# Kernel tuning notes

Hardware: AMD Instinct MI355X
Metric: run time of the kernel (lower is better)

Reference implementation:

```python
import jax, jax.numpy as jnp
import numpy as np

B, S, D = 2, 2048, 1024
H, Dh = 16, 64  # qkv_features=1024, head_dim=64
F = 1024        # out_features


def setup_inputs() -> dict:
    key = jax.random.key(0)
    ks = jax.random.split(key, 16)
    s = 0.02
    return {
        'inputs_q': jax.random.normal(ks[0], (B, S, D), jnp.float32),
        'inputs_kv': jax.random.normal(ks[1], (B, S, D), jnp.float32),
        'pos_embed': jax.random.normal(ks[2], (S, D), jnp.float32),
        'Wq': jax.random.normal(ks[3], (D, H, Dh), jnp.float32) * s,
        'bq': jnp.zeros((H, Dh), jnp.float32),
        'Wk': jax.random.normal(ks[4], (D, H, Dh), jnp.float32) * s,
        'bk': jnp.zeros((H, Dh), jnp.float32),
        'Wv': jax.random.normal(ks[5], (D, H, Dh), jnp.float32) * s,
        'bv': jnp.zeros((H, Dh), jnp.float32),
        'Wpos': jax.random.normal(ks[6], (D, H, Dh), jnp.float32) * s,
        'r_r_bias': jax.random.normal(ks[7], (H, Dh), jnp.float32) * s,
        'r_w_bias': jax.random.normal(ks[8], (H, Dh), jnp.float32) * s,
        'Wout': jax.random.normal(ks[9], (H, Dh, F), jnp.float32) * s,
        'bout': jnp.zeros((F,), jnp.float32),
    }


_roll_vmap = jax.vmap(jnp.roll, in_axes=(-2, 0, None), out_axes=-2)


def reference(inputs_q, inputs_kv, pos_embed, Wq, bq, Wk, bk, Wv, bv,
              Wpos, r_r_bias, r_w_bias, Wout, bout):
    # QKV projections: [B,S,D] x [D,H,Dh] -> [B,S,H,Dh]
    q = jnp.einsum('bsd,dhk->bshk', inputs_q, Wq) + bq
    k = jnp.einsum('bsd,dhk->bshk', inputs_kv, Wk) + bk
    v = jnp.einsum('bsd,dhk->bshk', inputs_kv, Wv) + bv
    # relative position embedding projection: [S,D] -> [S,H,Dh]
    r_pos = jnp.einsum('sd,dhk->shk', pos_embed, Wpos)

    q_len = q.shape[-3]
    depth = q.shape[-1]
    # content score + relative-position score, both [B,H,S,S]
    aw = jnp.einsum('bqhd,bkhd->bhqk', q + r_w_bias, k)
    aw_r = jnp.einsum('bqhd,khd->bhqk', q + r_r_bias, r_pos)
    # Transformer-XL relative shift: per query-row roll along key axis
    shifts = jnp.arange(0, q_len) - (q_len - 1)
    aw_r = _roll_vmap(aw_r, shifts, -1)
    aw = (aw + aw_r) / jnp.sqrt(depth).astype(aw.dtype)
    attn = jax.nn.softmax(aw, axis=-1)
    # weighted sum: [B,S,H,Dh]
    x = jnp.einsum('bhqk,bkhd->bqhd', attn, v)
    # output projection contracting (H,Dh)
    out = jnp.einsum('bqhd,hdf->bqf', x, Wout) + bout
    return out
```

## Files before the change

kernel.cpp:

```cpp
#include <hip/hip_runtime.h>
#include <hip/hip_bf16.h>
#include <hip/hip_fp16.h>


#define B_  2
#define S_  2048
#define D_  1024
#define H_  16
#define DH_ 64
#define HD_ 1024
#define F_  1024
#define N_  4096
#define KC_ 512
#define SP2 516
#define KQSC 0.1803368801111204f

typedef __attribute__((ext_vector_type(8))) short  short8;
typedef __attribute__((ext_vector_type(4))) float  floatx4;
typedef __attribute__((ext_vector_type(4))) unsigned int uintx4;

__device__ __forceinline__ unsigned short f2bf(float x) {
  unsigned u = __float_as_uint(x);
  u += 0x7FFFu + ((u >> 16) & 1u);
  return (unsigned short)(u >> 16);
}
__device__ __forceinline__ unsigned short f2h(float x) {
  __half h = __float2half(x);
  unsigned short u; __builtin_memcpy(&u, &h, 2);
  return u;
}
__device__ __forceinline__ float h2f(unsigned short u) {
  __half h; __builtin_memcpy(&h, &u, 2);
  return __half2float(h);
}

#define CQ_ (N_ * D_ / 4)
__global__ void cast_all(const float* __restrict__ sq, const float* __restrict__ skv,
                         const float* __restrict__ spos,
                         unsigned short* __restrict__ dq, unsigned short* __restrict__ dkv,
                         unsigned short* __restrict__ dpos) {
  int i = blockIdx.x * blockDim.x + threadIdx.x;
  const float* s; unsigned short* d; int off;
  if (i < CQ_)            { s = sq;   d = dq;   off = i; }
  else if (i < 2 * CQ_)   { s = skv;  d = dkv;  off = i - CQ_; }
  else                    { s = spos; d = dpos; off = i - 2 * CQ_; }
  float4 v = ((const float4*)s)[off];
  ushort4 o = make_ushort4(f2bf(v.x), f2bf(v.y), f2bf(v.z), f2bf(v.w));
  ((ushort4*)d)[off] = o;
}

struct TP5 { const float* s[5]; unsigned short* d[5]; };
__global__ void transpose_all(TP5 p) {
  __shared__ float t[32][33];
  const float* src = p.s[blockIdx.z];
  unsigned short* dst = p.d[blockIdx.z];
  int c0 = blockIdx.x * 32, r0 = blockIdx.y * 32;
  int tx = threadIdx.x, ty = threadIdx.y;
#pragma unroll
  for (int i = 0; i < 4; i++)
    t[ty + i * 8][tx] = src[(size_t)(r0 + ty + i * 8) * 1024 + c0 + tx];
  __syncthreads();
#pragma unroll
  for (int i = 0; i < 4; i++)
    dst[(size_t)(c0 + ty + i * 8) * 1024 + r0 + tx] = f2bf(t[tx][ty + i * 8]);
}

struct GSeg {
  const unsigned short* A; const unsigned short* Bt;
  const float* bias; const float* b2a; const float* b2b;
  unsigned short* outA; unsigned short* outB; float* outF;
  int mode; int bend;
};
struct GP { GSeg s[4]; };
__launch_bounds__(256, 2)
__global__ void gemm_bt(GP p, int Nn, int K) {
  __shared__ unsigned short As[128 * 64];
  __shared__ unsigned short Bs[128 * 64];
  int bx = blockIdx.x;
  GSeg g = p.s[0]; int base = 0;
  if (bx >= p.s[0].bend) { g = p.s[1]; base = p.s[0].bend; }
  if (bx >= p.s[1].bend) { g = p.s[2]; base = p.s[1].bend; }
  if (bx >= p.s[2].bend) { g = p.s[3]; base = p.s[2].bend; }
  bx -= base;
  int nb = Nn >> 7;
  int bm = bx / nb, bn = bx % nb;
  int tid = threadIdx.x;
  int lane = tid & 63, wv = tid >> 6;
  int wm = wv >> 1, wn = wv & 1;
  int lm = lane & 15, lg = lane >> 4;
  const unsigned short* Ab = g.A + (size_t)(bm * 128) * K;
  const unsigned short* Bb = g.Bt + (size_t)(bn * 128) * K;
  floatx4 acc[4][4];
#pragma unroll
  for (int i = 0; i < 4; i++)
#pragma unroll
    for (int j = 0; j < 4; j++) acc[i][j] = (floatx4){0.f, 0.f, 0.f, 0.f};

  int lr = tid >> 3;
  int lc = (tid & 7) * 8;
  for (int k0 = 0; k0 < K; k0 += 64) {
    __syncthreads();
#pragma unroll
    for (int i = 0; i < 4; i++) {
      int r = i * 32 + lr;
      *(uint4*)&As[r * 64 + lc] = *(const uint4*)&Ab[(size_t)r * K + k0 + lc];
      *(uint4*)&Bs[r * 64 + lc] = *(const uint4*)&Bb[(size_t)r * K + k0 + lc];
    }
    __syncthreads();
#pragma unroll
    for (int kk = 0; kk < 2; kk++) {
      short8 af[4], bf[4];
#pragma unroll
      for (int i = 0; i < 4; i++)
        af[i] = *(const short8*)&As[(wm * 64 + i * 16 + lm) * 64 + kk * 32 + lg * 8];
#pragma unroll
      for (int j = 0; j < 4; j++)
        bf[j] = *(const short8*)&Bs[(wn * 64 + j * 16 + lm) * 64 + kk * 32 + lg * 8];
#pragma unroll
      for (int i = 0; i < 4; i++)
#pragma unroll
        for (int j = 0; j < 4; j++)
          acc[i][j] = __builtin_amdgcn_mfma_f32_16x16x32_bf16(af[i], bf[j], acc[i][j], 0, 0, 0);
    }
  }
#pragma unroll
  for (int j = 0; j < 4; j++) {
    int col = bn * 128 + wn * 64 + j * 16 + lm;
    float bs = g.bias ? g.bias[col] : 0.f;
    float ba = g.b2a ? g.b2a[col] : 0.f;
    float bb = g.b2b ? g.b2b[col] : 0.f;
#pragma unroll
    for (int i = 0; i < 4; i++) {
      int row0 = bm * 128 + wm * 64 + i * 16 + lg * 4;
      if (g.mode == 4) {
        int s = row0 & 2047, bb2 = row0 >> 11;
        size_t vidx = (((size_t)bb2 * H_ + (col >> 6)) * 64 + (col & 63)) * (size_t)S_ + s;
        ushort4 o = make_ushort4(f2bf(acc[i][j][0] + bs), f2bf(acc[i][j][1] + bs),
                                 f2bf(acc[i][j][2] + bs), f2bf(acc[i][j][3] + bs));
        *(ushort4*)&g.outA[vidx] = o;
      } else {
#pragma unroll
        for (int r = 0; r < 4; r++) {
          float v = acc[i][j][r] + bs;
          size_t idx = (size_t)(row0 + r) * Nn + col;
          if (g.mode == 0)      g.outA[idx] = f2bf(v);
          else if (g.mode == 1) { g.outA[idx] = f2bf((v + ba) * KQSC); g.outB[idx] = f2bf((v + bb) * KQSC); }
          else                  g.outF[idx] = v;
        }
      }
    }
  }
}

__launch_bounds__(512, 4)
__global__ void attn_kernel(const unsigned short* __restrict__ qw,
                            const unsigned short* __restrict__ qr,
                            const unsigned short* __restrict__ kb,
                            const unsigned short* __restrict__ rb,
                            const unsigned short* __restrict__ vt,
                            unsigned short* __restrict__ xb) {
  __shared__ __align__(16) unsigned short sS[2][32 * SP2];
  __shared__ float sSum[8][32];
  __shared__ float sLinv[32];
  int bid = blockIdx.x;
  int l = ((bid & 7) << 8) | (bid >> 3);
  int qt = l & 63;
  int bh = l >> 6;
  int b = bh >> 4, h = bh & 15;
  int q0 = qt * 32;
  int tid = threadIdx.x;
  int lane = tid & 63, wv = tid >> 6;
  int lm = lane & 15, lg = lane >> 4;

  short8 bqw[2][2], bqr[2][2];
  const size_t qbase = (size_t)(b * S_ + q0) * HD_ + h * 64;
#pragma unroll
  for (int t = 0; t < 2; t++) {
    const unsigned short* p1 = qw + qbase + (size_t)(t * 16 + lm) * HD_ + lg * 8;
    const unsigned short* p2 = qr + qbase + (size_t)(t * 16 + lm) * HD_ + lg * 8;
    bqw[t][0] = *(const short8*)(p1);
    bqw[t][1] = *(const short8*)(p1 + 32);
    bqr[t][0] = *(const short8*)(p2);
    bqr[t][1] = *(const short8*)(p2 + 32);
  }

  floatx4 acc[2][4];
#pragma unroll
  for (int m = 0; m < 2; m++)
#pragma unroll
    for (int j = 0; j < 4; j++) acc[m][j] = (floatx4){0.f, 0.f, 0.f, 0.f};
  float s0 = 0.f, s1 = 0.f;

  const unsigned short* vb0 = vt + (size_t)(b * H_ + h) * 64 * S_;

  for (int c = 0; c < 4; c++) {
    unsigned short* S = sS[c & 1];
    int kc = c * KC_;
    for (int jt = wv; jt < 34; jt += 8) {
      int jrow = (kc - q0 - 32 + jt * 16 + lm) & 2047;
      const unsigned short* rp = rb + (size_t)jrow * HD_ + h * 64 + lg * 8;
      short8 a0 = *(const short8*)(rp);
      short8 a1 = *(const short8*)(rp + 32);
#pragma unroll
      for (int t = 0; t < 2; t++) {
        floatx4 c4 = (floatx4){0.f, 0.f, 0.f, 0.f};
        c4 = __builtin_amdgcn_mfma_f32_16x16x32_bf16(a0, bqr[t][0], c4, 0, 0, 0);
        c4 = __builtin_amdgcn_mfma_f32_16x16x32_bf16(a1, bqr[t][1], c4, 0, 0, 0);
        int q = t * 16 + lm;
        int ub = jt * 16 + lg * 4 + q - 31;
        unsigned short* row = &S[q * SP2];
        if (jt + t >= 2 && jt + t <= 32) {
#pragma unroll
          for (int r = 0; r < 4; r++) row[ub + r] = f2h(c4[r]);
        } else {
#pragma unroll
          for (int r = 0; r < 4; r++) {
            int u = ub + r;
            if ((unsigned)u < (unsigned)KC_) row[u] = f2h(c4[r]);
          }
        }
      }
    }
    __syncthreads();
#pragma unroll 2
    for (int kt = 0; kt < 4; kt++) {
      int u0 = wv * 64 + kt * 16;
      const unsigned short* kp = kb + (size_t)(b * S_ + kc + u0 + lm) * HD_ + h * 64 + lg * 8;
      short8 a0 = *(const short8*)(kp);
      short8 a1 = *(const short8*)(kp + 32);
#pragma unroll
      for (int t = 0; t < 2; t++) {
        floatx4 c4 = (floatx4){0.f, 0.f, 0.f, 0.f};
        c4 = __builtin_amdgcn_mfma_f32_16x16x32_bf16(a0, bqw[t][0], c4, 0, 0, 0);
        c4 = __builtin_amdgcn_mfma_f32_16x16x32_bf16(a1, bqw[t][1], c4, 0, 0, 0);
        int q = t * 16 + lm;
        unsigned short* pp = &S[q * SP2 + u0 + lg * 4];
        ushort4 Rv = *(const ushort4*)pp;
        float p0 = exp2f(c4[0] + h2f(Rv.x));
        float p1 = exp2f(c4[1] + h2f(Rv.y));
        float p2 = exp2f(c4[2] + h2f(Rv.z));
        float p3 = exp2f(c4[3] + h2f(Rv.w));
        float ps = (p0 + p1) + (p2 + p3);
        if (t == 0) s0 += ps; else s1 += ps;
        unsigned w0, w1;
        asm("v_cvt_pk_bf16_f32 %0, %1, %2" : "=v"(w0) : "v"(p0), "v"(p1));
        asm("v_cvt_pk_bf16_f32 %0, %1, %2" : "=v"(w1) : "v"(p2), "v"(p3));
        *(uint2*)pp = make_uint2(w0, w1);
      }
    }
#pragma unroll
    for (int s = 0; s < 2; s++) {
      int u0 = wv * 64 + s * 32;
      int e0 = lm * SP2 + u0 + lg * 8;
      int e1 = (16 + lm) * SP2 + u0 + lg * 8;
      uint2 x0 = *(const uint2*)&S[e0];
      uint2 x1 = *(const uint2*)&S[e0 + 4];
      uint2 y0 = *(const uint2*)&S[e1];
      uint2 y1 = *(const uint2*)&S[e1 + 4];
      uintx4 ua = {x0.x, x0.y, x1.x, x1.y};
      uintx4 ub = {y0.x, y0.y, y1.x, y1.y};
      short8 a0 = __builtin_bit_cast(short8, ua);
      short8 a1 = __builtin_bit_cast(short8, ub);
      const unsigned short* vp = vb0 + kc + u0 + lg * 8;
#pragma unroll
      for (int j = 0; j < 4; j++) {
        short8 bb = *(const short8*)&vp[(size_t)(j * 16 + lm) * S_];
        acc[0][j] = __builtin_amdgcn_mfma_f32_16x16x32_bf16(a0, bb, acc[0][j], 0, 0, 0);
        acc[1][j] = __builtin_amdgcn_mfma_f32_16x16x32_bf16(a1, bb, acc[1][j], 0, 0, 0);
      }
    }
  }
  s0 += __shfl_xor(s0, 16); s0 += __shfl_xor(s0, 32);
  s1 += __shfl_xor(s1, 16); s1 += __shfl_xor(s1, 32);
  if (lane < 16) { sSum[wv][lane] = s0; sSum[wv][16 + lane] = s1; }
  __syncthreads();
  if (tid < 32) {
    float t = 0.f;
#pragma unroll
    for (int w = 0; w < 8; w++) t += sSum[w][tid];
    sLinv[tid] = 1.f / t;
  }
  float* po = (float*)sS;
#pragma unroll
  for (int m = 0; m < 2; m++)
#pragma unroll
    for (int j = 0; j < 4; j++)
#pragma unroll
      for (int r = 0; r < 4; r++) {
        int q = m * 16 + lg * 4 + r;
        int dh = j * 16 + lm;
        po[wv * 2048 + q * 64 + dh] = acc[m][j][r];
      }
  __syncthreads();
  {
    int e = tid * 4;
    int q = e >> 6, dh = e & 63;
    float4 v = *(float4*)&po[e];
#pragma unroll
    for (int w = 1; w < 8; w++) {
      float4 u = *(float4*)&po[w * 2048 + e];
      v.x += u.x; v.y += u.y; v.z += u.z; v.w += u.w;
    }
    float li = sLinv[q];
    ushort4 o = make_ushort4(f2bf(v.x * li), f2bf(v.y * li), f2bf(v.z * li), f2bf(v.w * li));
    *(ushort4*)&xb[(size_t)(b * S_ + q0 + q) * HD_ + h * 64 + dh] = o;
  }
}

extern "C" void kernel_launch(void* const* d_in, const int* in_sizes, int n_in,
                              void* d_out, int out_size, void* d_ws, size_t ws_size,
                              hipStream_t stream) {
  const float* inputs_q  = (const float*)d_in[0];
  const float* inputs_kv = (const float*)d_in[1];
  const float* pos_embed = (const float*)d_in[2];
  const float* Wq   = (const float*)d_in[3];
  const float* bq   = (const float*)d_in[4];
  const float* Wk   = (const float*)d_in[5];
  const float* bk   = (const float*)d_in[6];
  const float* Wv   = (const float*)d_in[7];
  const float* bv   = (const float*)d_in[8];
  const float* Wpos = (const float*)d_in[9];
  const float* rrb  = (const float*)d_in[10];
  const float* rwb  = (const float*)d_in[11];
  const float* Wout = (const float*)d_in[12];
  const float* bout = (const float*)d_in[13];
  float* out = (float*)d_out;

  char* ws = (char*)d_ws;
  unsigned short* aq  = (unsigned short*)(ws);
  unsigned short* akv = (unsigned short*)(ws + ( 8u << 20));
  unsigned short* apo = (unsigned short*)(ws + (16u << 20));
  unsigned short* wqt = (unsigned short*)(ws + (20u << 20));
  unsigned short* wkt = (unsigned short*)(ws + (22u << 20));
  unsigned short* wvt = (unsigned short*)(ws + (24u << 20));
  unsigned short* wpt = (unsigned short*)(ws + (26u << 20));
  unsigned short* wot = (unsigned short*)(ws + (28u << 20));
  unsigned short* qwp = (unsigned short*)(ws + (30u << 20));
  unsigned short* qrp = (unsigned short*)(ws + (38u << 20));
  unsigned short* kbp = (unsigned short*)(ws + (46u << 20));
  unsigned short* vtp = (unsigned short*)(ws + (54u << 20));
  unsigned short* rbp = (unsigned short*)(ws + (62u << 20));
  unsigned short* xbp = aq;

  cast_all<<<10240, 256, 0, stream>>>(inputs_q, inputs_kv, pos_embed, aq, akv, apo);
  TP5 tp;
  tp.s[0] = Wq; tp.s[1] = Wk; tp.s[2] = Wv; tp.s[3] = Wpos; tp.s[4] = Wout;
  tp.d[0] = wqt; tp.d[1] = wkt; tp.d[2] = wvt; tp.d[3] = wpt; tp.d[4] = wot;
  transpose_all<<<dim3(32, 32, 5), dim3(32, 8), 0, stream>>>(tp);

  GP gp{};
  gp.s[0] = {aq,  wqt, bq,      rwb,     rrb,     qwp,     qrp,     nullptr, 1, 256};
  gp.s[1] = {apo, wpt, nullptr, nullptr, nullptr, rbp,     nullptr, nullptr, 0, 384};
  gp.s[2] = {akv, wkt, bk,      nullptr, nullptr, kbp,     nullptr, nullptr, 0, 640};
  gp.s[3] = {akv, wvt, bv,      nullptr, nullptr, vtp,     nullptr, nullptr, 4, 896};
  gemm_bt<<<896, 256, 0, stream>>>(gp, HD_, D_);

  attn_kernel<<<2048, 512, 0, stream>>>(qwp, qrp, kbp, rbp, vtp, xbp);

  GP go{};
  go.s[0] = {xbp, wot, bout, nullptr, nullptr, nullptr, nullptr, out, 2, 256};
  go.s[1] = {nullptr, nullptr, nullptr, nullptr, nullptr, nullptr, nullptr, nullptr, 0, 1 << 30};
  go.s[2] = go.s[1];
  go.s[3] = go.s[1];
  gemm_bt<<<256, 256, 0, stream>>>(go, F_, HD_);
}
```

Measured before the change: 405.9 us.

## Halve attention key chunk and split query halves across waves for occupancy

The attention kernel now processes keys in 256-wide chunks (8 chunks instead of 4), shrinking the shared-memory score buffer. Each wave owns one 16-row query half instead of both, which halves per-wave accumulator and Q-fragment registers. Launch bounds are raised to target 6 blocks per CU. The intent is higher occupancy for better latency hiding. In exchange there are more chunk iterations and barriers, and each K and V fragment load now feeds only one query half, so global and L2 load traffic per MFMA doubles.

Measured after the change: 625.7 us. +54.1%, slower.

```diff
diff --git a/kernel.cpp b/kernel.cpp
--- a/kernel.cpp
+++ b/kernel.cpp
@@ -11,8 +11,9 @@
 #define HD_ 1024
 #define F_  1024
 #define N_  4096
-#define KC_ 512
-#define SP2 516
+#define KC_ 256
+#define NCH 8
+#define SP2 260
 #define KQSC 0.1803368801111204f
 
 typedef __attribute__((ext_vector_type(8))) short  short8;
@@ -152,7 +153,7 @@
   }
 }
 
-__launch_bounds__(512, 4)
+__launch_bounds__(512, 6)
 __global__ void attn_kernel(const unsigned short* __restrict__ qw,
                             const unsigned short* __restrict__ qr,
                             const unsigned short* __restrict__ kb,
@@ -160,7 +161,7 @@
                             const unsigned short* __restrict__ vt,
                             unsigned short* __restrict__ xb) {
   __shared__ __align__(16) unsigned short sS[2][32 * SP2];
-  __shared__ float sSum[8][32];
+  __shared__ float sSum[8][16];
   __shared__ float sLinv[32];
   int bid = blockIdx.x;
   int l = ((bid & 7) << 8) | (bid >> 3);
@@ -171,134 +172,109 @@
   int tid = threadIdx.x;
   int lane = tid & 63, wv = tid >> 6;
   int lm = lane & 15, lg = lane >> 4;
-
-  short8 bqw[2][2], bqr[2][2];
-  const size_t qbase = (size_t)(b * S_ + q0) * HD_ + h * 64;
-#pragma unroll
-  for (int t = 0; t < 2; t++) {
-    const unsigned short* p1 = qw + qbase + (size_t)(t * 16 + lm) * HD_ + lg * 8;
-    const unsigned short* p2 = qr + qbase + (size_t)(t * 16 + lm) * HD_ + lg * 8;
-    bqw[t][0] = *(const short8*)(p1);
-    bqw[t][1] = *(const short8*)(p1 + 32);
-    bqr[t][0] = *(const short8*)(p2);
-    bqr[t][1] = *(const short8*)(p2 + 32);
-  }
-
-  floatx4 acc[2][4];
-#pragma unroll
-  for (int m = 0; m < 2; m++)
-#pragma unroll
-    for (int j = 0; j < 4; j++) acc[m][j] = (floatx4){0.f, 0.f, 0.f, 0.f};
-  float s0 = 0.f, s1 = 0.f;
+  int th = wv & 1, w2 = wv >> 1;
+
+  const size_t qbase = (size_t)(b * S_ + q0 + th * 16 + lm) * HD_ + h * 64 + lg * 8;
+  short8 bqw0 = *(const short8*)(qw + qbase);
+  short8 bqw1 = *(const short8*)(qw + qbase + 32);
+  short8 bqr0 = *(const short8*)(qr + qbase);
+  short8 bqr1 = *(const short8*)(qr + qbase + 32);
+
+  floatx4 acc[4];
+#pragma unroll
+  for (int j = 0; j < 4; j++) acc[j] = (floatx4){0.f, 0.f, 0.f, 0.f};
+  float s0 = 0.f;
 
   const unsigned short* vb0 = vt + (size_t)(b * H_ + h) * 64 * S_;
 
-  for (int c = 0; c < 4; c++) {
+  for (int c = 0; c < NCH; c++) {
     unsigned short* S = sS[c & 1];
     int kc = c * KC_;
-    for (int jt = wv; jt < 34; jt += 8) {
+    for (int jt = w2; jt < 18; jt += 4) {
       int jrow = (kc - q0 - 32 + jt * 16 + lm) & 2047;
       const unsigned short* rp = rb + (size_t)jrow * HD_ + h * 64 + lg * 8;
       short8 a0 = *(const short8*)(rp);
       short8 a1 = *(const short8*)(rp + 32);
-#pragma unroll
-      for (int t = 0; t < 2; t++) {
-        floatx4 c4 = (floatx4){0.f, 0.f, 0.f, 0.f};
-        c4 = __builtin_amdgcn_mfma_f32_16x16x32_bf16(a0, bqr[t][0], c4, 0, 0, 0);
-        c4 = __builtin_amdgcn_mfma_f32_16x16x32_bf16(a1, bqr[t][1], c4, 0, 0, 0);
-        int q = t * 16 + lm;
-        int ub = jt * 16 + lg * 4 + q - 31;
-        unsigned short* row = &S[q * SP2];
-        if (jt + t >= 2 && jt + t <= 32) {
-#pragma unroll
-          for (int r = 0; r < 4; r++) row[ub + r] = f2h(c4[r]);
-        } else {
-#pragma unroll
-          for (int r = 0; r < 4; r++) {
-            int u = ub + r;
-            if ((unsigned)u < (unsigned)KC_) row[u] = f2h(c4[r]);
-          }
+      floatx4 c4 = (floatx4){0.f, 0.f, 0.f, 0.f};
+      c4 = __builtin_amdgcn_mfma_f32_16x16x32_bf16(a0, bqr0, c4, 0, 0, 0);
+      c4 = __builtin_amdgcn_mfma_f32_16x16x32_bf16(a1, bqr1, c4, 0, 0, 0);
+      int q = th * 16 + lm;
+      int ub = jt * 16 + lg * 4 + q - 31;
+      unsigned short* row = &S[q * SP2];
+      if (jt + th >= 2 && jt + th <= 16) {
+#pragma unroll
+        for (int r = 0; r < 4; r++) row[ub + r] = f2h(c4[r]);
+      } else {
+#pragma unroll
+        for (int r = 0; r < 4; r++) {
+          int u = ub + r;
+          if ((unsigned)u < (unsigned)KC_) row[u] = f2h(c4[r]);
         }
       }
     }
     __syncthreads();
-#pragma unroll 2
+#pragma unroll
     for (int kt = 0; kt < 4; kt++) {
-      int u0 = wv * 64 + kt * 16;
+      int u0 = w2 * 64 + kt * 16;
       const unsigned short* kp = kb + (size_t)(b * S_ + kc + u0 + lm) * HD_ + h * 64 + lg * 8;
       short8 a0 = *(const short8*)(kp);
       short8 a1 = *(const short8*)(kp + 32);
-#pragma unroll
-      for (int t = 0; t < 2; t++) {
-        floatx4 c4 = (floatx4){0.f, 0.f, 0.f, 0.f};
-        c4 = __builtin_amdgcn_mfma_f32_16x16x32_bf16(a0, bqw[t][0], c4, 0, 0, 0);
-        c4 = __builtin_amdgcn_mfma_f32_16x16x32_bf16(a1, bqw[t][1], c4, 0, 0, 0);
-        int q = t * 16 + lm;
-        unsigned short* pp = &S[q * SP2 + u0 + lg * 4];
-        ushort4 Rv = *(const ushort4*)pp;
-        float p0 = exp2f(c4[0] + h2f(Rv.x));
-        float p1 = exp2f(c4[1] + h2f(Rv.y));
-        float p2 = exp2f(c4[2] + h2f(Rv.z));
-        float p3 = exp2f(c4[3] + h2f(Rv.w));
-        float ps = (p0 + p1) + (p2 + p3);
-        if (t == 0) s0 += ps; else s1 += ps;
-        unsigned w0, w1;
-        asm("v_cvt_pk_bf16_f32 %0, %1, %2" : "=v"(w0) : "v"(p0), "v"(p1));
-        asm("v_cvt_pk_bf16_f32 %0, %1, %2" : "=v"(w1) : "v"(p2), "v"(p3));
-        *(uint2*)pp = make_uint2(w0, w1);
-      }
+      floatx4 c4 = (floatx4){0.f, 0.f, 0.f, 0.f};
+      c4 = __builtin_amdgcn_mfma_f32_16x16x32_bf16(a0, bqw0, c4, 0, 0, 0);
+      c4 = __builtin_amdgcn_mfma_f32_16x16x32_bf16(a1, bqw1, c4, 0, 0, 0);
+      int q = th * 16 + lm;
+      unsigned short* pp = &S[q * SP2 + u0 + lg * 4];
+      ushort4 Rv = *(const ushort4*)pp;
+      float p0 = exp2f(c4[0] + h2f(Rv.x));
+      float p1 = exp2f(c4[1] + h2f(Rv.y));
+      float p2 = exp2f(c4[2] + h2f(Rv.z));
+      float p3 = exp2f(c4[3] + h2f(Rv.w));
+      s0 += (p0 + p1) + (p2 + p3);
+      unsigned w0, w1;
+      asm("v_cvt_pk_bf16_f32 %0, %1, %2" : "=v"(w0) : "v"(p0), "v"(p1));
+      asm("v_cvt_pk_bf16_f32 %0, %1, %2" : "=v"(w1) : "v"(p2), "v"(p3));
+      *(uint2*)pp = make_uint2(w0, w1);
     }
 #pragma unroll
     for (int s = 0; s < 2; s++) {
-      int u0 = wv * 64 + s * 32;
-      int e0 = lm * SP2 + u0 + lg * 8;
-      int e1 = (16 + lm) * SP2 + u0 + lg * 8;
+      int u0 = w2 * 64 + s * 32;
+      int e0 = (th * 16 + lm) * SP2 + u0 + lg * 8;
       uint2 x0 = *(const uint2*)&S[e0];
       uint2 x1 = *(const uint2*)&S[e0 + 4];
-      uint2 y0 = *(const uint2*)&S[e1];
-      uint2 y1 = *(const uint2*)&S[e1 + 4];
       uintx4 ua = {x0.x, x0.y, x1.x, x1.y};
-      uintx4 ub = {y0.x, y0.y, y1.x, y1.y};
       short8 a0 = __builtin_bit_cast(short8, ua);
-      short8 a1 = __builtin_bit_cast(short8, ub);
       const unsigned short* vp = vb0 + kc + u0 + lg * 8;
 #pragma unroll
       for (int j = 0; j < 4; j++) {
         short8 bb = *(const short8*)&vp[(size_t)(j * 16 + lm) * S_];
-        acc[0][j] = __builtin_amdgcn_mfma_f32_16x16x32_bf16(a0, bb, acc[0][j], 0, 0, 0);
-        acc[1][j] = __builtin_amdgcn_mfma_f32_16x16x32_bf16(a1, bb, acc[1][j], 0, 0, 0);
+        acc[j] = __builtin_amdgcn_mfma_f32_16x16x32_bf16(a0, bb, acc[j], 0, 0, 0);
       }
     }
   }
   s0 += __shfl_xor(s0, 16); s0 += __shfl_xor(s0, 32);
-  s1 += __shfl_xor(s1, 16); s1 += __shfl_xor(s1, 32);
-  if (lane < 16) { sSum[wv][lane] = s0; sSum[wv][16 + lane] = s1; }
+  if (lane < 16) sSum[wv][lane] = s0;
   __syncthreads();
   if (tid < 32) {
     float t = 0.f;
 #pragma unroll
-    for (int w = 0; w < 8; w++) t += sSum[w][tid];
+    for (int i = 0; i < 4; i++) t += sSum[2 * i + (tid >> 4)][tid & 15];
     sLinv[tid] = 1.f / t;
   }
   float* po = (float*)sS;
 #pragma unroll
-  for (int m = 0; m < 2; m++)
-#pragma unroll
-    for (int j = 0; j < 4; j++)
-#pragma unroll
-      for (int r = 0; r < 4; r++) {
-        int q = m * 16 + lg * 4 + r;
-        int dh = j * 16 + lm;
-        po[wv * 2048 + q * 64 + dh] = acc[m][j][r];
-      }
+  for (int j = 0; j < 4; j++)
+#pragma unroll
+    for (int r = 0; r < 4; r++)
+      po[wv * 1024 + (lg * 4 + r) * 64 + j * 16 + lm] = acc[j][r];
   __syncthreads();
   {
     int e = tid * 4;
     int q = e >> 6, dh = e & 63;
-    float4 v = *(float4*)&po[e];
-#pragma unroll
-    for (int w = 1; w < 8; w++) {
-      float4 u = *(float4*)&po[w * 2048 + e];
+    int th2 = q >> 4, lq = q & 15;
+    float4 v = *(float4*)&po[th2 * 1024 + lq * 64 + dh];
+#pragma unroll
+    for (int i = 1; i < 4; i++) {
+      float4 u = *(float4*)&po[(2 * i + th2) * 1024 + lq * 64 + dh];
       v.x += u.x; v.y += u.y; v.z += u.z; v.w += u.w;
     }
     float li = sLinv[q];
```

## Fuse prep kernels and software-pipeline global loads in attention loop

Applied to the files above, without the earlier changes.

Merges the input cast and weight transpose kernels into one launch to save a kernel launch. In the attention kernel, the relative-position row loads are double-buffered against the MFMA/stores, K tiles are prefetched across the barrier, and V tiles are loaded up front. MFMA sections are wrapped in s_setprio raises. This hides global-memory latency behind compute at the cost of more live registers, which could lower occupancy or cause spills.

Result: slower. 540.9 us (+33.3%).

```diff
diff --git a/kernel.cpp b/kernel.cpp
--- a/kernel.cpp
+++ b/kernel.cpp
@@ -35,34 +35,39 @@
 }
 
 #define CQ_ (N_ * D_ / 4)
-__global__ void cast_all(const float* __restrict__ sq, const float* __restrict__ skv,
-                         const float* __restrict__ spos,
-                         unsigned short* __restrict__ dq, unsigned short* __restrict__ dkv,
-                         unsigned short* __restrict__ dpos) {
-  int i = blockIdx.x * blockDim.x + threadIdx.x;
-  const float* s; unsigned short* d; int off;
-  if (i < CQ_)            { s = sq;   d = dq;   off = i; }
-  else if (i < 2 * CQ_)   { s = skv;  d = dkv;  off = i - CQ_; }
-  else                    { s = spos; d = dpos; off = i - 2 * CQ_; }
-  float4 v = ((const float4*)s)[off];
-  ushort4 o = make_ushort4(f2bf(v.x), f2bf(v.y), f2bf(v.z), f2bf(v.w));
-  ((ushort4*)d)[off] = o;
-}
-
-struct TP5 { const float* s[5]; unsigned short* d[5]; };
-__global__ void transpose_all(TP5 p) {
+#define CAST_BLKS 10240
+struct PrepP {
+  const float* sq; const float* skv; const float* spos;
+  unsigned short* dq; unsigned short* dkv; unsigned short* dpos;
+  const float* ts[5]; unsigned short* td[5];
+};
+__global__ void prep_all(PrepP p) {
   __shared__ float t[32][33];
-  const float* src = p.s[blockIdx.z];
-  unsigned short* dst = p.d[blockIdx.z];
-  int c0 = blockIdx.x * 32, r0 = blockIdx.y * 32;
-  int tx = threadIdx.x, ty = threadIdx.y;
-#pragma unroll
-  for (int i = 0; i < 4; i++)
-    t[ty + i * 8][tx] = src[(size_t)(r0 + ty + i * 8) * 1024 + c0 + tx];
-  __syncthreads();
-#pragma unroll
-  for (int i = 0; i < 4; i++)
-    dst[(size_t)(c0 + ty + i * 8) * 1024 + r0 + tx] = f2bf(t[tx][ty + i * 8]);
+  int bid = blockIdx.x;
+  int tid = threadIdx.x;
+  if (bid < CAST_BLKS) {
+    int i = bid * 256 + tid;
+    const float* s; unsigned short* d; int off;
+    if (i < CQ_)            { s = p.sq;   d = p.dq;   off = i; }
+    else if (i < 2 * CQ_)   { s = p.skv;  d = p.dkv;  off = i - CQ_; }
+    else                    { s = p.spos; d = p.dpos; off = i - 2 * CQ_; }
+    float4 v = ((const float4*)s)[off];
+    ((ushort4*)d)[off] = make_ushort4(f2bf(v.x), f2bf(v.y), f2bf(v.z), f2bf(v.w));
+  } else {
+    int b2 = bid - CAST_BLKS;
+    int z = b2 >> 10, y = (b2 >> 5) & 31, x = b2 & 31;
+    const float* src = p.ts[z];
+    unsigned short* dst = p.td[z];
+    int c0 = x * 32, r0 = y * 32;
+    int tx = tid & 31, ty = tid >> 5;
+#pragma unroll
+    for (int i = 0; i < 4; i++)
+      t[ty + i * 8][tx] = src[(size_t)(r0 + ty + i * 8) * 1024 + c0 + tx];
+    __syncthreads();
+#pragma unroll
+    for (int i = 0; i < 4; i++)
+      dst[(size_t)(c0 + ty + i * 8) * 1024 + r0 + tx] = f2bf(t[tx][ty + i * 8]);
+  }
 }
 
 struct GSeg {
@@ -196,16 +201,21 @@
   for (int c = 0; c < 4; c++) {
     unsigned short* S = sS[c & 1];
     int kc = c * KC_;
-    for (int jt = wv; jt < 34; jt += 8) {
+
+    auto rload = [&](int jt, short8& a0, short8& a1) {
       int jrow = (kc - q0 - 32 + jt * 16 + lm) & 2047;
       const unsigned short* rp = rb + (size_t)jrow * HD_ + h * 64 + lg * 8;
-      short8 a0 = *(const short8*)(rp);
-      short8 a1 = *(const short8*)(rp + 32);
+      a0 = *(const short8*)(rp);
+      a1 = *(const short8*)(rp + 32);
+    };
+    auto rstore = [&](int jt, short8 a0, short8 a1) {
 #pragma unroll
       for (int t = 0; t < 2; t++) {
         floatx4 c4 = (floatx4){0.f, 0.f, 0.f, 0.f};
+        __builtin_amdgcn_s_setprio(1);
         c4 = __builtin_amdgcn_mfma_f32_16x16x32_bf16(a0, bqr[t][0], c4, 0, 0, 0);
         c4 = __builtin_amdgcn_mfma_f32_16x16x32_bf16(a1, bqr[t][1], c4, 0, 0, 0);
+        __builtin_amdgcn_s_setprio(0);
         int q = t * 16 + lm;
         int ub = jt * 16 + lg * 4 + q - 31;
         unsigned short* row = &S[q * SP2];
@@ -220,19 +230,44 @@
           }
         }
       }
-    }
+    };
+    {
+      short8 ra0, ra1, rc0, rc1;
+      rload(wv, ra0, ra1);
+      rload(wv + 8, rc0, rc1);
+      rstore(wv, ra0, ra1);
+      rload(wv + 16, ra0, ra1);
+      rstore(wv + 8, rc0, rc1);
+      rload(wv + 24, rc0, rc1);
+      rstore(wv + 16, ra0, ra1);
+      if (wv < 2) {
+        rload(wv + 32, ra0, ra1);
+        rstore(wv + 24, rc0, rc1);
+        rstore(wv + 32, ra0, ra1);
+      } else {
+        rstore(wv + 24, rc0, rc1);
+      }
+    }
+    const unsigned short* kp = kb + (size_t)(b * S_ + kc + wv * 64 + lm) * HD_ + h * 64 + lg * 8;
+    short8 k0a = *(const short8*)(kp);
+    short8 k0b = *(const short8*)(kp + 32);
+    short8 k1a = *(const short8*)(kp + 16 * HD_);
+    short8 k1b = *(const short8*)(kp + 16 * HD_ + 32);
     __syncthreads();
-#pragma unroll 2
-    for (int kt = 0; kt < 4; kt++) {
+    short8 k2a = *(const short8*)(kp + 32 * HD_);
+    short8 k2b = *(const short8*)(kp + 32 * HD_ + 32);
+    short8 k3a = *(const short8*)(kp + 48 * HD_);
+    short8 k3b = *(const short8*)(kp + 48 * HD_ + 32);
+
+    auto bphase = [&](short8 a0, short8 a1, int kt) {
       int u0 = wv * 64 + kt * 16;
-      const unsigned short* kp = kb + (size_t)(b * S_ + kc + u0 + lm) * HD_ + h * 64 + lg * 8;
-      short8 a0 = *(const short8*)(kp);
-      short8 a1 = *(const short8*)(kp + 32);
 #pragma unroll
       for (int t = 0; t < 2; t++) {
         floatx4 c4 = (floatx4){0.f, 0.f, 0.f, 0.f};
+        __builtin_amdgcn_s_setprio(1);
         c4 = __builtin_amdgcn_mfma_f32_16x16x32_bf16(a0, bqw[t][0], c4, 0, 0, 0);
         c4 = __builtin_amdgcn_mfma_f32_16x16x32_bf16(a1, bqw[t][1], c4, 0, 0, 0);
+        __builtin_amdgcn_s_setprio(0);
         int q = t * 16 + lm;
         unsigned short* pp = &S[q * SP2 + u0 + lg * 4];
         ushort4 Rv = *(const ushort4*)pp;
@@ -247,27 +282,47 @@
         asm("v_cvt_pk_bf16_f32 %0, %1, %2" : "=v"(w1) : "v"(p2), "v"(p3));
         *(uint2*)pp = make_uint2(w0, w1);
       }
-    }
-#pragma unroll
-    for (int s = 0; s < 2; s++) {
-      int u0 = wv * 64 + s * 32;
+    };
+    bphase(k0a, k0b, 0);
+    bphase(k1a, k1b, 1);
+    bphase(k2a, k2b, 2);
+    bphase(k3a, k3b, 3);
+
+    {
+      int u0 = wv * 64;
+      const unsigned short* vp = vb0 + kc + u0 + lg * 8;
+      short8 v0[4], v1[4];
+#pragma unroll
+      for (int j = 0; j < 4; j++) {
+        v0[j] = *(const short8*)&vp[(size_t)(j * 16 + lm) * S_];
+        v1[j] = *(const short8*)&vp[(size_t)(j * 16 + lm) * S_ + 32];
+      }
       int e0 = lm * SP2 + u0 + lg * 8;
       int e1 = (16 + lm) * SP2 + u0 + lg * 8;
-      uint2 x0 = *(const uint2*)&S[e0];
-      uint2 x1 = *(const uint2*)&S[e0 + 4];
-      uint2 y0 = *(const uint2*)&S[e1];
-      uint2 y1 = *(const uint2*)&S[e1 + 4];
-      uintx4 ua = {x0.x, x0.y, x1.x, x1.y};
-      uintx4 ub = {y0.x, y0.y, y1.x, y1.y};
-      short8 a0 = __builtin_bit_cast(short8, ua);
-      short8 a1 = __builtin_bit_cast(short8, ub);
-      const unsigned short* vp = vb0 + kc + u0 + lg * 8;
+      uint2 x0 = *(const uint2*)&S[e0],      x1 = *(const uint2*)&S[e0 + 4];
+      uint2 x2 = *(const uint2*)&S[e0 + 32], x3 = *(const uint2*)&S[e0 + 36];
+      uint2 y0 = *(const uint2*)&S[e1],      y1 = *(const uint2*)&S[e1 + 4];
+      uint2 y2 = *(const uint2*)&S[e1 + 32], y3 = *(const uint2*)&S[e1 + 36];
+      uintx4 up00 = {x0.x, x0.y, x1.x, x1.y};
+      uintx4 up01 = {y0.x, y0.y, y1.x, y1.y};
+      uintx4 up10 = {x2.x, x2.y, x3.x, x3.y};
+      uintx4 up11 = {y2.x, y2.y, y3.x, y3.y};
+      short8 p00 = __builtin_bit_cast(short8, up00);
+      short8 p01 = __builtin_bit_cast(short8, up01);
+      short8 p10 = __builtin_bit_cast(short8, up10);
+      short8 p11 = __builtin_bit_cast(short8, up11);
+      __builtin_amdgcn_s_setprio(1);
 #pragma unroll
       for (int j = 0; j < 4; j++) {
-        short8 bb = *(const short8*)&vp[(size_t)(j * 16 + lm) * S_];
-        acc[0][j] = __builtin_amdgcn_mfma_f32_16x16x32_bf16(a0, bb, acc[0][j], 0, 0, 0);
-        acc[1][j] = __builtin_amdgcn_mfma_f32_16x16x32_bf16(a1, bb, acc[1][j], 0, 0, 0);
-      }
+        acc[0][j] = __builtin_amdgcn_mfma_f32_16x16x32_bf16(p00, v0[j], acc[0][j], 0, 0, 0);
+        acc[1][j] = __builtin_amdgcn_mfma_f32_16x16x32_bf16(p01, v0[j], acc[1][j], 0, 0, 0);
+      }
+#pragma unroll
+      for (int j = 0; j < 4; j++) {
+        acc[0][j] = __builtin_amdgcn_mfma_f32_16x16x32_bf16(p10, v1[j], acc[0][j], 0, 0, 0);
+        acc[1][j] = __builtin_amdgcn_mfma_f32_16x16x32_bf16(p11, v1[j], acc[1][j], 0, 0, 0);
+      }
+      __builtin_amdgcn_s_setprio(0);
     }
   }
   s0 += __shfl_xor(s0, 16); s0 += __shfl_xor(s0, 32);
@@ -342,11 +397,12 @@
   unsigned short* rbp = (unsigned short*)(ws + (62u << 20));
   unsigned short* xbp = aq;
 
-  cast_all<<<10240, 256, 0, stream>>>(inputs_q, inputs_kv, pos_embed, aq, akv, apo);
-  TP5 tp;
-  tp.s[0] = Wq; tp.s[1] = Wk; tp.s[2] = Wv; tp.s[3] = Wpos; tp.s[4] = Wout;
-  tp.d[0] = wqt; tp.d[1] = wkt; tp.d[2] = wvt; tp.d[3] = wpt; tp.d[4] = wot;
-  transpose_all<<<dim3(32, 32, 5), dim3(32, 8), 0, stream>>>(tp);
+  PrepP pp;
+  pp.sq = inputs_q; pp.skv = inputs_kv; pp.spos = pos_embed;
+  pp.dq = aq; pp.dkv = akv; pp.dpos = apo;
+  pp.ts[0] = Wq; pp.ts[1] = Wk; pp.ts[2] = Wv; pp.ts[3] = Wpos; pp.ts[4] = Wout;
+  pp.td[0] = wqt; pp.td[1] = wkt; pp.td[2] = wvt; pp.td[3] = wpt; pp.td[4] = wot;
+  prep_all<<<CAST_BLKS + 5120, 256, 0, stream>>>(pp);
 
   GP gp{};
   gp.s[0] = {aq,  wqt, bq,      rwb,     rrb,     qwp,     qrp,     nullptr, 1, 256};
```

## Single-buffer attention score tile, reload Q per chunk, merge prep kernels

Applied to the files above, without the earlier changes.

Attention kernel drops the double-buffered LDS score tile and adds a trailing barrier per chunk. Q fragments are reloaded from global memory per chunk instead of being held in registers, and unrolling is reduced, so more workgroups fit per CU (launch bounds raised to 6). The final cross-wave reduction reuses half the LDS by having waves 4-7 accumulate into waves 0-3's slots. The cast and transpose prep kernels are fused into one launch to save a kernel launch. The cost is an extra barrier per chunk, repeated Q loads and less instruction-level parallelism.

Measured after the change: 505.4 us. +24.5%, slower.

```diff
diff --git a/kernel.cpp b/kernel.cpp
--- a/kernel.cpp
+++ b/kernel.cpp
@@ -35,34 +35,39 @@
 }
 
 #define CQ_ (N_ * D_ / 4)
-__global__ void cast_all(const float* __restrict__ sq, const float* __restrict__ skv,
-                         const float* __restrict__ spos,
-                         unsigned short* __restrict__ dq, unsigned short* __restrict__ dkv,
-                         unsigned short* __restrict__ dpos) {
-  int i = blockIdx.x * blockDim.x + threadIdx.x;
-  const float* s; unsigned short* d; int off;
-  if (i < CQ_)            { s = sq;   d = dq;   off = i; }
-  else if (i < 2 * CQ_)   { s = skv;  d = dkv;  off = i - CQ_; }
-  else                    { s = spos; d = dpos; off = i - 2 * CQ_; }
-  float4 v = ((const float4*)s)[off];
-  ushort4 o = make_ushort4(f2bf(v.x), f2bf(v.y), f2bf(v.z), f2bf(v.w));
-  ((ushort4*)d)[off] = o;
-}
-
-struct TP5 { const float* s[5]; unsigned short* d[5]; };
-__global__ void transpose_all(TP5 p) {
+#define CAST_BLKS 10240
+struct PrepP {
+  const float* sq; const float* skv; const float* spos;
+  unsigned short* dq; unsigned short* dkv; unsigned short* dpos;
+  const float* ts[5]; unsigned short* td[5];
+};
+__global__ void prep_all(PrepP p) {
   __shared__ float t[32][33];
-  const float* src = p.s[blockIdx.z];
-  unsigned short* dst = p.d[blockIdx.z];
-  int c0 = blockIdx.x * 32, r0 = blockIdx.y * 32;
-  int tx = threadIdx.x, ty = threadIdx.y;
-#pragma unroll
-  for (int i = 0; i < 4; i++)
-    t[ty + i * 8][tx] = src[(size_t)(r0 + ty + i * 8) * 1024 + c0 + tx];
-  __syncthreads();
-#pragma unroll
-  for (int i = 0; i < 4; i++)
-    dst[(size_t)(c0 + ty + i * 8) * 1024 + r0 + tx] = f2bf(t[tx][ty + i * 8]);
+  int bid = blockIdx.x;
+  int tid = threadIdx.x;
+  if (bid < CAST_BLKS) {
+    int i = bid * 256 + tid;
+    const float* s; unsigned short* d; int off;
+    if (i < CQ_)            { s = p.sq;   d = p.dq;   off = i; }
+    else if (i < 2 * CQ_)   { s = p.skv;  d = p.dkv;  off = i - CQ_; }
+    else                    { s = p.spos; d = p.dpos; off = i - 2 * CQ_; }
+    float4 v = ((const float4*)s)[off];
+    ((ushort4*)d)[off] = make_ushort4(f2bf(v.x), f2bf(v.y), f2bf(v.z), f2bf(v.w));
+  } else {
+    int b2 = bid - CAST_BLKS;
+    int z = b2 >> 10, y = (b2 >> 5) & 31, x = b2 & 31;
+    const float* src = p.ts[z];
+    unsigned short* dst = p.td[z];
+    int c0 = x * 32, r0 = y * 32;
+    int tx = tid & 31, ty = tid >> 5;
+#pragma unroll
+    for (int i = 0; i < 4; i++)
+      t[ty + i * 8][tx] = src[(size_t)(r0 + ty + i * 8) * 1024 + c0 + tx];
+    __syncthreads();
+#pragma unroll
+    for (int i = 0; i < 4; i++)
+      dst[(size_t)(c0 + ty + i * 8) * 1024 + r0 + tx] = f2bf(t[tx][ty + i * 8]);
+  }
 }
 
 struct GSeg {
@@ -152,14 +157,14 @@
   }
 }
 
-__launch_bounds__(512, 4)
+__launch_bounds__(512, 6)
 __global__ void attn_kernel(const unsigned short* __restrict__ qw,
                             const unsigned short* __restrict__ qr,
                             const unsigned short* __restrict__ kb,
                             const unsigned short* __restrict__ rb,
                             const unsigned short* __restrict__ vt,
                             unsigned short* __restrict__ xb) {
-  __shared__ __align__(16) unsigned short sS[2][32 * SP2];
+  __shared__ __align__(16) unsigned short sS[32 * SP2];
   __shared__ float sSum[8][32];
   __shared__ float sLinv[32];
   int bid = blockIdx.x;
@@ -172,18 +177,6 @@
   int lane = tid & 63, wv = tid >> 6;
   int lm = lane & 15, lg = lane >> 4;
 
-  short8 bqw[2][2], bqr[2][2];
-  const size_t qbase = (size_t)(b * S_ + q0) * HD_ + h * 64;
-#pragma unroll
-  for (int t = 0; t < 2; t++) {
-    const unsigned short* p1 = qw + qbase + (size_t)(t * 16 + lm) * HD_ + lg * 8;
-    const unsigned short* p2 = qr + qbase + (size_t)(t * 16 + lm) * HD_ + lg * 8;
-    bqw[t][0] = *(const short8*)(p1);
-    bqw[t][1] = *(const short8*)(p1 + 32);
-    bqr[t][0] = *(const short8*)(p2);
-    bqr[t][1] = *(const short8*)(p2 + 32);
-  }
-
   floatx4 acc[2][4];
 #pragma unroll
   for (int m = 0; m < 2; m++)
@@ -192,10 +185,18 @@
   float s0 = 0.f, s1 = 0.f;
 
   const unsigned short* vb0 = vt + (size_t)(b * H_ + h) * 64 * S_;
+  const size_t qfo = (size_t)(b * S_ + q0) * HD_ + h * 64;
 
   for (int c = 0; c < 4; c++) {
-    unsigned short* S = sS[c & 1];
     int kc = c * KC_;
+    asm volatile("" ::: "memory");
+    short8 bq[2][2];
+#pragma unroll
+    for (int t = 0; t < 2; t++) {
+      const unsigned short* p2 = qr + qfo + (size_t)(t * 16 + lm) * HD_ + lg * 8;
+      bq[t][0] = *(const short8*)(p2);
+      bq[t][1] = *(const short8*)(p2 + 32);
+    }
     for (int jt = wv; jt < 34; jt += 8) {
       int jrow = (kc - q0 - 32 + jt * 16 + lm) & 2047;
       const unsigned short* rp = rb + (size_t)jrow * HD_ + h * 64 + lg * 8;
@@ -204,11 +205,11 @@
 #pragma unroll
       for (int t = 0; t < 2; t++) {
         floatx4 c4 = (floatx4){0.f, 0.f, 0.f, 0.f};
-        c4 = __builtin_amdgcn_mfma_f32_16x16x32_bf16(a0, bqr[t][0], c4, 0, 0, 0);
-        c4 = __builtin_amdgcn_mfma_f32_16x16x32_bf16(a1, bqr[t][1], c4, 0, 0, 0);
+        c4 = __builtin_amdgcn_mfma_f32_16x16x32_bf16(a0, bq[t][0], c4, 0, 0, 0);
+        c4 = __builtin_amdgcn_mfma_f32_16x16x32_bf16(a1, bq[t][1], c4, 0, 0, 0);
         int q = t * 16 + lm;
         int ub = jt * 16 + lg * 4 + q - 31;
-        unsigned short* row = &S[q * SP2];
+        unsigned short* row = &sS[q * SP2];
         if (jt + t >= 2 && jt + t <= 32) {
 #pragma unroll
           for (int r = 0; r < 4; r++) row[ub + r] = f2h(c4[r]);
@@ -222,7 +223,14 @@
       }
     }
     __syncthreads();
-#pragma unroll 2
+    asm volatile("" ::: "memory");
+#pragma unroll
+    for (int t = 0; t < 2; t++) {
+      const unsigned short* p1 = qw + qfo + (size_t)(t * 16 + lm) * HD_ + lg * 8;
+      bq[t][0] = *(const short8*)(p1);
+      bq[t][1] = *(const short8*)(p1 + 32);
+    }
+#pragma unroll 1
     for (int kt = 0; kt < 4; kt++) {
       int u0 = wv * 64 + kt * 16;
       const unsigned short* kp = kb + (size_t)(b * S_ + kc + u0 + lm) * HD_ + h * 64 + lg * 8;
@@ -231,10 +239,10 @@
 #pragma unroll
       for (int t = 0; t < 2; t++) {
         floatx4 c4 = (floatx4){0.f, 0.f, 0.f, 0.f};
-        c4 = __builtin_amdgcn_mfma_f32_16x16x32_bf16(a0, bqw[t][0], c4, 0, 0, 0);
-        c4 = __builtin_amdgcn_mfma_f32_16x16x32_bf16(a1, bqw[t][1], c4, 0, 0, 0);
+        c4 = __builtin_amdgcn_mfma_f32_16x16x32_bf16(a0, bq[t][0], c4, 0, 0, 0);
+        c4 = __builtin_amdgcn_mfma_f32_16x16x32_bf16(a1, bq[t][1], c4, 0, 0, 0);
         int q = t * 16 + lm;
-        unsigned short* pp = &S[q * SP2 + u0 + lg * 4];
+        unsigned short* pp = &sS[q * SP2 + u0 + lg * 4];
         ushort4 Rv = *(const ushort4*)pp;
         float p0 = exp2f(c4[0] + h2f(Rv.x));
         float p1 = exp2f(c4[1] + h2f(Rv.y));
@@ -248,15 +256,15 @@
         *(uint2*)pp = make_uint2(w0, w1);
       }
     }
-#pragma unroll
+#pragma unroll 1
     for (int s = 0; s < 2; s++) {
       int u0 = wv * 64 + s * 32;
       int e0 = lm * SP2 + u0 + lg * 8;
       int e1 = (16 + lm) * SP2 + u0 + lg * 8;
-      uint2 x0 = *(const uint2*)&S[e0];
-      uint2 x1 = *(const uint2*)&S[e0 + 4];
-      uint2 y0 = *(const uint2*)&S[e1];
-      uint2 y1 = *(const uint2*)&S[e1 + 4];
+      uint2 x0 = *(const uint2*)&sS[e0];
+      uint2 x1 = *(const uint2*)&sS[e0 + 4];
+      uint2 y0 = *(const uint2*)&sS[e1];
+      uint2 y1 = *(const uint2*)&sS[e1 + 4];
       uintx4 ua = {x0.x, x0.y, x1.x, x1.y};
       uintx4 ub = {y0.x, y0.y, y1.x, y1.y};
       short8 a0 = __builtin_bit_cast(short8, ua);
@@ -269,10 +277,24 @@
         acc[1][j] = __builtin_amdgcn_mfma_f32_16x16x32_bf16(a1, bb, acc[1][j], 0, 0, 0);
       }
     }
+    __syncthreads();
   }
   s0 += __shfl_xor(s0, 16); s0 += __shfl_xor(s0, 32);
   s1 += __shfl_xor(s1, 16); s1 += __shfl_xor(s1, 32);
   if (lane < 16) { sSum[wv][lane] = s0; sSum[wv][16 + lane] = s1; }
+  float* po = (float*)sS;
+  if (wv < 4) {
+#pragma unroll
+    for (int m = 0; m < 2; m++)
+#pragma unroll
+      for (int j = 0; j < 4; j++)
+#pragma unroll
+        for (int r = 0; r < 4; r++) {
+          int q = m * 16 + lg * 4 + r;
+          int dh = j * 16 + lm;
+          po[wv * 2048 + q * 64 + dh] = acc[m][j][r];
+        }
+  }
   __syncthreads();
   if (tid < 32) {
     float t = 0.f;
@@ -280,25 +302,26 @@
     for (int w = 0; w < 8; w++) t += sSum[w][tid];
     sLinv[tid] = 1.f / t;
   }
-  float* po = (float*)sS;
-#pragma unroll
-  for (int m = 0; m < 2; m++)
-#pragma unroll
-    for (int j = 0; j < 4; j++)
-#pragma unroll
-      for (int r = 0; r < 4; r++) {
-        int q = m * 16 + lg * 4 + r;
-        int dh = j * 16 + lm;
-        po[wv * 2048 + q * 64 + dh] = acc[m][j][r];
-      }
+  if (wv >= 4) {
+#pragma unroll
+    for (int m = 0; m < 2; m++)
+#pragma unroll
+      for (int j = 0; j < 4; j++)
+#pragma unroll
+        for (int r = 0; r < 4; r++) {
+          int q = m * 16 + lg * 4 + r;
+          int dh = j * 16 + lm;
+          po[(wv - 4) * 2048 + q * 64 + dh] += acc[m][j][r];
+        }
+  }
   __syncthreads();
   {
     int e = tid * 4;
     int q = e >> 6, dh = e & 63;
     float4 v = *(float4*)&po[e];
 #pragma unroll
-    for (int w = 1; w < 8; w++) {
-      float4 u = *(float4*)&po[w * 2048 + e];
+    for (int i = 1; i < 4; i++) {
+      float4 u = *(float4*)&po[i * 2048 + e];
       v.x += u.x; v.y += u.y; v.z += u.z; v.w += u.w;
     }
     float li = sLinv[q];
@@ -342,11 +365,12 @@
   unsigned short* rbp = (unsigned short*)(ws + (62u << 20));
   unsigned short* xbp = aq;
 
-  cast_all<<<10240, 256, 0, stream>>>(inputs_q, inputs_kv, pos_embed, aq, akv, apo);
-  TP5 tp;
-  tp.s[0] = Wq; tp.s[1] = Wk; tp.s[2] = Wv; tp.s[3] = Wpos; tp.s[4] = Wout;
-  tp.d[0] = wqt; tp.d[1] = wkt; tp.d[2] = wvt; tp.d[3] = wpt; tp.d[4] = wot;
-  transpose_all<<<dim3(32, 32, 5), dim3(32, 8), 0, stream>>>(tp);
+  PrepP pp;
+  pp.sq = inputs_q; pp.skv = inputs_kv; pp.spos = pos_embed;
+  pp.dq = aq; pp.dkv = akv; pp.dpos = apo;
+  pp.ts[0] = Wq; pp.ts[1] = Wk; pp.ts[2] = Wv; pp.ts[3] = Wpos; pp.ts[4] = Wout;
+  pp.td[0] = wqt; pp.td[1] = wkt; pp.td[2] = wvt; pp.td[3] = wpt; pp.td[4] = wot;
+  prep_all<<<CAST_BLKS + 5120, 256, 0, stream>>>(pp);
 
   GP gp{};
   gp.s[0] = {aq,  wqt, bq,      rwb,     rrb,     qwp,     qrp,     nullptr, 1, 256};
```
